# Kernel tuning notes

Measured on AMD Instinct MI355X. Metric: run time of the kernel, lower is better.

Reference implementation:

```python
import jax, jax.numpy as jnp
import numpy as np

B, STEPS, EMB = 2048, 512, 128
HID, CATE = 256, 2
IN_GRU = EMB + STEPS + 1  # input_size + self.length (length+1)


def setup_inputs() -> dict:
    key = jax.random.key(0)
    ks = jax.random.split(key, 7)
    s_ih = 1.0 / np.sqrt(HID)
    inputs = jax.random.normal(ks[0], (B, STEPS, EMB), dtype=jnp.float32)
    W_ih = jax.random.uniform(ks[1], (3 * HID, IN_GRU), jnp.float32, -s_ih, s_ih)
    W_hh = jax.random.uniform(ks[2], (3 * HID, HID), jnp.float32, -s_ih, s_ih)
    b_ih = jax.random.uniform(ks[3], (3 * HID,), jnp.float32, -s_ih, s_ih)
    b_hh = jax.random.uniform(ks[4], (3 * HID,), jnp.float32, -s_ih, s_ih)
    s_cf = 1.0 / np.sqrt(HID)
    W_cf = jax.random.uniform(ks[5], (CATE, HID), jnp.float32, -s_cf, s_cf)
    b_cf = jax.random.uniform(ks[6], (CATE,), jnp.float32, -s_cf, s_cf)
    return {"inputs": inputs, "W_ih": W_ih, "W_hh": W_hh, "b_ih": b_ih,
            "b_hh": b_hh, "W_cf": W_cf, "b_cf": b_cf}


def _gru_cell(x, h, W_ih, W_hh, b_ih, b_hh):
    # torch.nn.GRUCell math: gates ordered (r, z, n)
    gi = x @ W_ih.T + b_ih
    gh = h @ W_hh.T + b_hh
    i_r, i_z, i_n = jnp.split(gi, 3, axis=1)
    h_r, h_z, h_n = jnp.split(gh, 3, axis=1)
    r = jax.nn.sigmoid(i_r + h_r)
    z = jax.nn.sigmoid(i_z + h_z)
    n = jnp.tanh(i_n + r * h_n)
    return (1.0 - z) * n + z * h


def reference(inputs, W_ih, W_hh, b_ih, b_hh, W_cf, b_cf):
    # Eval-mode forward (self.training == False): greedy argmax action.
    b, steps, _ = inputs.shape
    hid = W_hh.shape[1]
    xs = jnp.swapaxes(inputs, 0, 1)  # [steps, b, emb]

    def step(carry, x):
        h, tag = carry
        tag_onehot = jax.nn.one_hot(tag, steps + 1, dtype=x.dtype)  # [b, steps+1]
        i_t = jnp.concatenate([x, tag_onehot], axis=1)
        h = _gru_cell(i_t, h, W_ih, W_hh, b_ih, b_hh)
        probs = jax.nn.softmax(h @ W_cf.T + b_cf, axis=1)  # [b, cate]
        action = jnp.argmax(probs, axis=1)                  # [b]
        pi = jnp.take_along_axis(probs, action[:, None], axis=1)[:, 0]
        tag = tag + action.astype(tag.dtype)  # cumulative sum of actions so far
        return (h, tag), (action.astype(x.dtype), pi)

    h0 = jnp.zeros((b, hid), dtype=inputs.dtype)
    tag0 = jnp.zeros((b,), dtype=jnp.int32)
    _, (outs, pis) = jax.lax.scan(step, (h0, tag0), xs)
    return jnp.swapaxes(outs, 0, 1), jnp.swapaxes(pis, 0, 1)  # each [b, steps]
```

## Files before the change

### kernel.cpp

```cpp
#include <hip/hip_runtime.h>
#include <math.h>

#define BATCH 2048
#define STEPS 512
#define EMB   128
#define HID   256
#define INGRU 641

#define WXP_OFF  49152
#define WCOL_OFF 294912

__global__ void prep_weights(const float* __restrict__ W_ih,
                             const float* __restrict__ W_hh,
                             float* __restrict__ ws) {
    const int idx = blockIdx.x * 256 + threadIdx.x;
    float4* __restrict__ Wp = (float4*)ws;
    if (idx < 49152) {
        const int k4 = idx / 768, rem = idx % 768;
        const int d = rem / 3, g = rem % 3;
        Wp[idx] = *(const float4*)(W_hh + ((size_t)(g * 256 + d)) * HID + 4 * k4);
    }
    if (idx < 24576) {
        const int k4 = idx / 768, rem = idx % 768;
        const int d = rem / 3, g = rem % 3;
        const float* src = W_ih + ((size_t)(g * 256 + d)) * INGRU + 4 * k4;
        Wp[WXP_OFF + idx] = make_float4(src[0], src[1], src[2], src[3]);
    }
    if (idx < 513 * 768) {
        const int c = idx / 768, gg = idx % 768;
        ws[WCOL_OFF + (size_t)c * 768 + gg] = W_ih[(size_t)gg * INGRU + EMB + c];
    }
}

#define FMA8(ACC, S, A, B) do {                                           \
    ACC[0] = fmaf(S, (A).x, ACC[0]); ACC[1] = fmaf(S, (A).y, ACC[1]);     \
    ACC[2] = fmaf(S, (A).z, ACC[2]); ACC[3] = fmaf(S, (A).w, ACC[3]);     \
    ACC[4] = fmaf(S, (B).x, ACC[4]); ACC[5] = fmaf(S, (B).y, ACC[5]);     \
    ACC[6] = fmaf(S, (B).z, ACC[6]); ACC[7] = fmaf(S, (B).w, ACC[7]);     \
} while (0)

#define K1(A0, A1, A2, S0, S1, S2, HP, OFF) do {                          \
    const float4 hA = *(const float4*)((HP) + (OFF));                     \
    const float4 hB = *(const float4*)((HP) + (OFF) + 4);                 \
    FMA8(A0, S0, hA, hB); FMA8(A1, S1, hA, hB); FMA8(A2, S2, hA, hB);     \
} while (0)

#define CONS(A0, A1, A2, W0, W1, W2, HP) do {                             \
    K1(A0, A1, A2, (W0).x, (W1).x, (W2).x, HP, 0);                        \
    K1(A0, A1, A2, (W0).y, (W1).y, (W2).y, HP, 12);                       \
    K1(A0, A1, A2, (W0).z, (W1).z, (W2).z, HP, 24);                       \
    K1(A0, A1, A2, (W0).w, (W1).w, (W2).w, HP, 36);                       \
} while (0)

__device__ __forceinline__ float bcast_lane(float v, int lane) {
    return __uint_as_float(
        __builtin_amdgcn_readlane(__float_as_uint(v), lane));
}

#define RLK(W0, W1, W2, E, M, LB) do {                                    \
    const float we0 = (W0).E, we1 = (W1).E, we2 = (W2).E;                 \
    _Pragma("unroll")                                                     \
    for (int j = 0; j < 8; ++j) {                                         \
        const float sv = bcast_lane(hreg[M], (LB) + j);                   \
        aH0[j] = fmaf(we0, sv, aH0[j]);                                   \
        aH1[j] = fmaf(we1, sv, aH1[j]);                                   \
        aH2[j] = fmaf(we2, sv, aH2[j]);                                   \
    }                                                                     \
} while (0)

__global__ __launch_bounds__(512, 2) void gru_policy(
    const float* __restrict__ X,
    const float* __restrict__ ws,
    const float* __restrict__ b_ih,
    const float* __restrict__ b_hh,
    const float* __restrict__ W_cf,
    const float* __restrict__ b_cf,
    float* __restrict__ out)
{
    const float4* __restrict__ Wp   = (const float4*)ws;
    const float*  __restrict__ Wcol = ws + WCOL_OFF;

    __shared__ __align__(16) float h_lds[2][HID][12];
    __shared__ __align__(16) float x_lds[EMB][12];
    __shared__ float ah_lds[3][8][256];
    __shared__ __align__(16) float red[8][8];

    const int t     = threadIdx.x;
    const int xduty = (t < 256);
    const int d     = t & 255;
    const int wv    = t >> 6;
    const int lane  = t & 63;
    const size_t r0 = (size_t)blockIdx.x * 8;
    const size_t xstride = (size_t)STEPS * EMB;

    const float bh0 = b_hh[d], bh1 = b_hh[d + 256], bh2 = b_hh[d + 512];
    const float bi0 = b_ih[d], bi1 = b_ih[d + 256], bi2 = b_ih[d + 512];
    const float wcf0 = W_cf[d], wcf1 = W_cf[256 + d];
    const float bc0 = b_cf[0], bc1 = b_cf[1];

    int   tags[8];
    float hp[8];
    #pragma unroll
    for (int j = 0; j < 8; ++j) { tags[j] = 0; hp[j] = 0.0f; }

    for (int i = t; i < HID * 8; i += 512) h_lds[0][i >> 3][i & 7] = 0.0f;
    if (xduty) {
        #pragma unroll
        for (int q = 0; q < 4; ++q) {
            const int i = d + 256 * q, row = i >> 7, col = i & 127;
            x_lds[col][row] = X[(r0 + row) * xstride + col];
        }
    }
    __syncthreads();

    int cur = 0;
    for (int s = 0; s < STEPS; ++s) {
        float aI0[8], aI1[8], aI2[8];
        float xn[4];
        if (!xduty) {
            float aH0[8], aH1[8], aH2[8];
            #pragma unroll
            for (int j = 0; j < 8; ++j) { aH0[j] = bh0; aH1[j] = bh1; aH2[j] = bh2; }

            float hreg[16];
            {
                const int qg = lane >> 3, jj = lane & 7;
                #pragma unroll
                for (int m = 0; m < 16; ++m)
                    hreg[m] = h_lds[cur][128 + 16 * qg + m][jj];
            }

            __builtin_amdgcn_s_setprio(1);
            {
                const float* hb = &h_lds[cur][0][0];
                const float4* wp = Wp + (size_t)d * 3;
                float4 a0 = wp[0], a1 = wp[1], a2 = wp[2]; wp += 768;
                float4 b0 = wp[0], b1 = wp[1], b2 = wp[2]; wp += 768;
                #pragma unroll 2
                for (int it = 0; it < 30; it += 2) {
                    const float4 c0 = wp[0], c1 = wp[1], c2 = wp[2]; wp += 768;
                    const float4 e0 = wp[0], e1 = wp[1], e2 = wp[2]; wp += 768;
                    CONS(aH0, aH1, aH2, a0, a1, a2, hb + it * 48);
                    CONS(aH0, aH1, aH2, b0, b1, b2, hb + it * 48 + 48);
                    a0 = c0; a1 = c1; a2 = c2; b0 = e0; b1 = e1; b2 = e2;
                }
                CONS(aH0, aH1, aH2, a0, a1, a2, hb + 30 * 48);
                CONS(aH0, aH1, aH2, b0, b1, b2, hb + 31 * 48);
            }
            #pragma unroll 1
            for (int q = 0; q < 8; ++q) {
                const int lb = q << 3;
                const float4* wq = Wp + (size_t)(32 + 4 * q) * 768 + (size_t)d * 3;
                #pragma unroll
                for (int mg = 0; mg < 4; ++mg) {
                    const float4 w0 = wq[mg * 768];
                    const float4 w1 = wq[mg * 768 + 1];
                    const float4 w2 = wq[mg * 768 + 2];
                    RLK(w0, w1, w2, x, 4 * mg + 0, lb);
                    RLK(w0, w1, w2, y, 4 * mg + 1, lb);
                    RLK(w0, w1, w2, z, 4 * mg + 2, lb);
                    RLK(w0, w1, w2, w, 4 * mg + 3, lb);
                }
            }
            __builtin_amdgcn_s_setprio(0);
            #pragma unroll
            for (int j = 0; j < 8; ++j) {
                ah_lds[0][j][d] = aH0[j];
                ah_lds[1][j][d] = aH1[j];
                ah_lds[2][j][d] = aH2[j];
            }
        } else {
            #pragma unroll
            for (int j = 0; j < 8; ++j) {
                const size_t tg = (size_t)tags[j] * 768;
                aI0[j] = bi0 + Wcol[tg + d];
                aI1[j] = bi1 + Wcol[tg + 256 + d];
                aI2[j] = bi2 + Wcol[tg + 512 + d];
            }
            if (s + 1 < STEPS) {
                #pragma unroll
                for (int q = 0; q < 4; ++q) {
                    const int i = d + 256 * q, row = i >> 7, col = i & 127;
                    xn[q] = X[(r0 + row) * xstride + (size_t)(s + 1) * EMB + col];
                }
            }
            const float* xb = &x_lds[0][0];
            const float4* wq = Wp + WXP_OFF + (size_t)d * 3;
            float4 a0 = wq[0], a1 = wq[1], a2 = wq[2]; wq += 768;
            float4 b0 = wq[0], b1 = wq[1], b2 = wq[2]; wq += 768;
            #pragma unroll 2
            for (int it = 0; it < 30; it += 2) {
                const float4 c0 = wq[0], c1 = wq[1], c2 = wq[2]; wq += 768;
                const float4 e0 = wq[0], e1 = wq[1], e2 = wq[2]; wq += 768;
                CONS(aI0, aI1, aI2, a0, a1, a2, xb + it * 48);
                CONS(aI0, aI1, aI2, b0, b1, b2, xb + it * 48 + 48);
                a0 = c0; a1 = c1; a2 = c2; b0 = e0; b1 = e1; b2 = e2;
            }
            CONS(aI0, aI1, aI2, a0, a1, a2, xb + 30 * 48);
            CONS(aI0, aI1, aI2, b0, b1, b2, xb + 31 * 48);
        }
        __syncthreads();

        if (xduty) {
            float p0[8], p1[8], hn[8];
            #pragma unroll
            for (int j = 0; j < 8; ++j) {
                const float ah0 = ah_lds[0][j][d];
                const float ah1 = ah_lds[1][j][d];
                const float ah2 = ah_lds[2][j][d];
                const float rr = 1.0f / (1.0f + expf(-(aI0[j] + ah0)));
                const float zz = 1.0f / (1.0f + expf(-(aI1[j] + ah1)));
                const float nn = tanhf(aI2[j] + rr * ah2);
                const float h  = (1.0f - zz) * nn + zz * hp[j];
                hp[j] = h;
                hn[j] = h;
                p0[j] = h * wcf0;
                p1[j] = h * wcf1;
            }
            *(float4*)(&h_lds[cur ^ 1][d][0]) =
                make_float4(hn[0], hn[1], hn[2], hn[3]);
            *(float4*)(&h_lds[cur ^ 1][d][4]) =
                make_float4(hn[4], hn[5], hn[6], hn[7]);
            #pragma unroll
            for (int m = 32; m >= 1; m >>= 1) {
                #pragma unroll
                for (int j = 0; j < 8; ++j) {
                    p0[j] += __shfl_xor(p0[j], m, 64);
                    p1[j] += __shfl_xor(p1[j], m, 64);
                }
            }
            if (lane == 0) {
                #pragma unroll
                for (int j = 0; j < 8; ++j) {
                    red[j][wv * 2]     = p0[j];
                    red[j][wv * 2 + 1] = p1[j];
                }
            }
            if (s + 1 < STEPS) {
                #pragma unroll
                for (int q = 0; q < 4; ++q) {
                    const int i = d + 256 * q, row = i >> 7, col = i & 127;
                    x_lds[col][row] = xn[q];
                }
            }
        }
        __syncthreads();

        if (xduty) {
            #pragma unroll
            for (int j = 0; j < 8; ++j) {
                const float4 rA = *(const float4*)&red[j][0];
                const float4 rB = *(const float4*)&red[j][4];
                float l0 = bc0; l0 += rA.x; l0 += rA.z; l0 += rB.x; l0 += rB.z;
                float l1 = bc1; l1 += rA.y; l1 += rA.w; l1 += rB.y; l1 += rB.w;
                const int act = (l1 > l0) ? 1 : 0;
                tags[j] += act;
                if (t == j) {
                    const float mx = fmaxf(l0, l1);
                    const float e0 = expf(l0 - mx), e1 = expf(l1 - mx);
                    const float pi = (act ? e1 : e0) / (e0 + e1);
                    const size_t row = r0 + j;
                    out[row * STEPS + s] = (float)act;
                    out[(size_t)BATCH * STEPS + row * STEPS + s] = pi;
                }
            }
        }
        cur ^= 1;
    }
}

extern "C" void kernel_launch(void* const* d_in, const int* in_sizes, int n_in,
                              void* d_out, int out_size, void* d_ws, size_t ws_size,
                              hipStream_t stream) {
    const float* X    = (const float*)d_in[0];
    const float* W_ih = (const float*)d_in[1];
    const float* W_hh = (const float*)d_in[2];
    const float* b_ih = (const float*)d_in[3];
    const float* b_hh = (const float*)d_in[4];
    const float* W_cf = (const float*)d_in[5];
    const float* b_cf = (const float*)d_in[6];
    float* out = (float*)d_out;
    float* ws  = (float*)d_ws;

    prep_weights<<<1539, 256, 0, stream>>>(W_ih, W_hh, ws);
    gru_policy<<<BATCH / 8, 512, 0, stream>>>(X, ws, b_ih, b_hh, W_cf, b_cf, out);
}
```

Baseline: 10.06 ms.

## Read x directly from global memory and drop readlane split in hidden matvec

The x-projection threads now load input rows straight from global memory as broadcast float4 loads per batch row, instead of staging the next step's x tile through LDS with a prefetch. The hidden-side threads drop the readlane-broadcast path used for the upper half of the hidden state and run the whole 256-wide reduction through the LDS-based CONS loop. This removes the x_lds buffer and the readlane work, but puts global load latency on the x path every step and raises LDS read traffic on the h path.

```diff
diff --git a/kernel.cpp b/kernel.cpp
--- a/kernel.cpp
+++ b/kernel.cpp
@@ -52,19 +52,21 @@
     K1(A0, A1, A2, (W0).w, (W1).w, (W2).w, HP, 36);                       \
 } while (0)
 
-__device__ __forceinline__ float bcast_lane(float v, int lane) {
-    return __uint_as_float(
-        __builtin_amdgcn_readlane(__float_as_uint(v), lane));
-}
-
-#define RLK(W0, W1, W2, E, M, LB) do {                                    \
-    const float we0 = (W0).E, we1 = (W1).E, we2 = (W2).E;                 \
+__device__ __forceinline__ float f4e(const float4 v, int e) {
+    return e == 0 ? v.x : e == 1 ? v.y : e == 2 ? v.z : v.w;
+}
+
+#define XCONS(W0, W1, W2, XQ) do {                                        \
     _Pragma("unroll")                                                     \
-    for (int j = 0; j < 8; ++j) {                                         \
-        const float sv = bcast_lane(hreg[M], (LB) + j);                   \
-        aH0[j] = fmaf(we0, sv, aH0[j]);                                   \
-        aH1[j] = fmaf(we1, sv, aH1[j]);                                   \
-        aH2[j] = fmaf(we2, sv, aH2[j]);                                   \
+    for (int e = 0; e < 4; ++e) {                                         \
+        const float w0e = f4e(W0, e), w1e = f4e(W1, e), w2e = f4e(W2, e); \
+        _Pragma("unroll")                                                 \
+        for (int j = 0; j < 8; ++j) {                                     \
+            const float xv = f4e(XQ[j], e);                               \
+            aI0[j] = fmaf(w0e, xv, aI0[j]);                               \
+            aI1[j] = fmaf(w1e, xv, aI1[j]);                               \
+            aI2[j] = fmaf(w2e, xv, aI2[j]);                               \
+        }                                                                 \
     }                                                                     \
 } while (0)
 
@@ -81,7 +83,6 @@
     const float*  __restrict__ Wcol = ws + WCOL_OFF;
 
     __shared__ __align__(16) float h_lds[2][HID][12];
-    __shared__ __align__(16) float x_lds[EMB][12];
     __shared__ float ah_lds[3][8][256];
     __shared__ __align__(16) float red[8][8];
 
@@ -103,66 +104,39 @@
     #pragma unroll
     for (int j = 0; j < 8; ++j) { tags[j] = 0; hp[j] = 0.0f; }
 
+    const float* xb[8];
+    #pragma unroll
+    for (int j = 0; j < 8; ++j) xb[j] = X + (r0 + j) * xstride;
+
     for (int i = t; i < HID * 8; i += 512) h_lds[0][i >> 3][i & 7] = 0.0f;
-    if (xduty) {
-        #pragma unroll
-        for (int q = 0; q < 4; ++q) {
-            const int i = d + 256 * q, row = i >> 7, col = i & 127;
-            x_lds[col][row] = X[(r0 + row) * xstride + col];
-        }
-    }
     __syncthreads();
 
     int cur = 0;
     for (int s = 0; s < STEPS; ++s) {
         float aI0[8], aI1[8], aI2[8];
-        float xn[4];
         if (!xduty) {
             float aH0[8], aH1[8], aH2[8];
             #pragma unroll
             for (int j = 0; j < 8; ++j) { aH0[j] = bh0; aH1[j] = bh1; aH2[j] = bh2; }
 
-            float hreg[16];
-            {
-                const int qg = lane >> 3, jj = lane & 7;
-                #pragma unroll
-                for (int m = 0; m < 16; ++m)
-                    hreg[m] = h_lds[cur][128 + 16 * qg + m][jj];
-            }
+            const float* hb = &h_lds[cur][0][0];
+            const float4* wp = Wp + (size_t)d * 3;
+            float4 a0 = wp[0], a1 = wp[1], a2 = wp[2]; wp += 768;
+            float4 b0 = wp[0], b1 = wp[1], b2 = wp[2]; wp += 768;
 
             __builtin_amdgcn_s_setprio(1);
-            {
-                const float* hb = &h_lds[cur][0][0];
-                const float4* wp = Wp + (size_t)d * 3;
-                float4 a0 = wp[0], a1 = wp[1], a2 = wp[2]; wp += 768;
-                float4 b0 = wp[0], b1 = wp[1], b2 = wp[2]; wp += 768;
-                #pragma unroll 2
-                for (int it = 0; it < 30; it += 2) {
-                    const float4 c0 = wp[0], c1 = wp[1], c2 = wp[2]; wp += 768;
-                    const float4 e0 = wp[0], e1 = wp[1], e2 = wp[2]; wp += 768;
-                    CONS(aH0, aH1, aH2, a0, a1, a2, hb + it * 48);
-                    CONS(aH0, aH1, aH2, b0, b1, b2, hb + it * 48 + 48);
-                    a0 = c0; a1 = c1; a2 = c2; b0 = e0; b1 = e1; b2 = e2;
-                }
-                CONS(aH0, aH1, aH2, a0, a1, a2, hb + 30 * 48);
-                CONS(aH0, aH1, aH2, b0, b1, b2, hb + 31 * 48);
-            }
-            #pragma unroll 1
-            for (int q = 0; q < 8; ++q) {
-                const int lb = q << 3;
-                const float4* wq = Wp + (size_t)(32 + 4 * q) * 768 + (size_t)d * 3;
-                #pragma unroll
-                for (int mg = 0; mg < 4; ++mg) {
-                    const float4 w0 = wq[mg * 768];
-                    const float4 w1 = wq[mg * 768 + 1];
-                    const float4 w2 = wq[mg * 768 + 2];
-                    RLK(w0, w1, w2, x, 4 * mg + 0, lb);
-                    RLK(w0, w1, w2, y, 4 * mg + 1, lb);
-                    RLK(w0, w1, w2, z, 4 * mg + 2, lb);
-                    RLK(w0, w1, w2, w, 4 * mg + 3, lb);
-                }
-            }
+            #pragma unroll 2
+            for (int it = 0; it < 62; it += 2) {
+                const float4 c0 = wp[0], c1 = wp[1], c2 = wp[2]; wp += 768;
+                const float4 e0 = wp[0], e1 = wp[1], e2 = wp[2]; wp += 768;
+                CONS(aH0, aH1, aH2, a0, a1, a2, hb + it * 48);
+                CONS(aH0, aH1, aH2, b0, b1, b2, hb + it * 48 + 48);
+                a0 = c0; a1 = c1; a2 = c2; b0 = e0; b1 = e1; b2 = e2;
+            }
+            CONS(aH0, aH1, aH2, a0, a1, a2, hb + 62 * 48);
+            CONS(aH0, aH1, aH2, b0, b1, b2, hb + 63 * 48);
             __builtin_amdgcn_s_setprio(0);
+
             #pragma unroll
             for (int j = 0; j < 8; ++j) {
                 ah_lds[0][j][d] = aH0[j];
@@ -177,27 +151,17 @@
                 aI1[j] = bi1 + Wcol[tg + 256 + d];
                 aI2[j] = bi2 + Wcol[tg + 512 + d];
             }
-            if (s + 1 < STEPS) {
+            const size_t so = (size_t)s * EMB;
+            const float4* wq = Wp + WXP_OFF + (size_t)d * 3;
+            #pragma unroll 4
+            for (int k4 = 0; k4 < 32; ++k4) {
+                const float4 w0 = wq[0], w1 = wq[1], w2 = wq[2]; wq += 768;
+                float4 xq[8];
                 #pragma unroll
-                for (int q = 0; q < 4; ++q) {
-                    const int i = d + 256 * q, row = i >> 7, col = i & 127;
-                    xn[q] = X[(r0 + row) * xstride + (size_t)(s + 1) * EMB + col];
-                }
-            }
-            const float* xb = &x_lds[0][0];
-            const float4* wq = Wp + WXP_OFF + (size_t)d * 3;
-            float4 a0 = wq[0], a1 = wq[1], a2 = wq[2]; wq += 768;
-            float4 b0 = wq[0], b1 = wq[1], b2 = wq[2]; wq += 768;
-            #pragma unroll 2
-            for (int it = 0; it < 30; it += 2) {
-                const float4 c0 = wq[0], c1 = wq[1], c2 = wq[2]; wq += 768;
-                const float4 e0 = wq[0], e1 = wq[1], e2 = wq[2]; wq += 768;
-                CONS(aI0, aI1, aI2, a0, a1, a2, xb + it * 48);
-                CONS(aI0, aI1, aI2, b0, b1, b2, xb + it * 48 + 48);
-                a0 = c0; a1 = c1; a2 = c2; b0 = e0; b1 = e1; b2 = e2;
-            }
-            CONS(aI0, aI1, aI2, a0, a1, a2, xb + 30 * 48);
-            CONS(aI0, aI1, aI2, b0, b1, b2, xb + 31 * 48);
+                for (int j = 0; j < 8; ++j)
+                    xq[j] = *(const float4*)(xb[j] + so + 4 * k4);
+                XCONS(w0, w1, w2, xq);
+            }
         }
         __syncthreads();
 
@@ -221,6 +185,7 @@
                 make_float4(hn[0], hn[1], hn[2], hn[3]);
             *(float4*)(&h_lds[cur ^ 1][d][4]) =
                 make_float4(hn[4], hn[5], hn[6], hn[7]);
+
             #pragma unroll
             for (int m = 32; m >= 1; m >>= 1) {
                 #pragma unroll
@@ -234,13 +199,6 @@
                 for (int j = 0; j < 8; ++j) {
                     red[j][wv * 2]     = p0[j];
                     red[j][wv * 2 + 1] = p1[j];
-                }
-            }
-            if (s + 1 < STEPS) {
-                #pragma unroll
-                for (int q = 0; q < 4; ++q) {
-                    const int i = d + 256 * q, row = i >> 7, col = i & 127;
-                    x_lds[col][row] = xn[q];
                 }
             }
         }
```

Result: slower. 16.78 ms (+66.9%).
